# Kernel tuning notes

Measured on AMD Instinct MI355X. Metric: run time of the kernel, lower is better.

## Reference

```python
import jax, jax.numpy as jnp
import numpy as np

B, H, F, Z, T = 8192, 256, 128, 64, 43
STEPS = T - 3


def setup_inputs() -> dict:
    key = jax.random.key(0)
    ks = jax.random.split(key, 24)
    def nrm(k, shape, s=0.05):
        return (jax.random.normal(k, shape) * s).astype(jnp.float32)
    inp = {}
    inp["h_i"] = nrm(ks[0], (B, H), 1.0)                      # encoder context state
    t = jax.random.uniform(ks[1], (B, T)) * T                  # event timestamps, sorted
    inp["input_t"] = jnp.sort(t, axis=1).astype(jnp.float32)
    inp["eps_inf"] = jax.random.normal(ks[2], (STEPS, B, Z), dtype=jnp.float32)
    inp["eps_prior"] = jax.random.normal(ks[3], (STEPS, B, Z), dtype=jnp.float32)
    in_dim = Z + H + F
    inp["Wx"] = nrm(ks[4], (in_dim, 4 * H))
    inp["Wh"] = nrm(ks[5], (H, 4 * H))
    inp["b_lstm"] = jnp.zeros((4 * H,), jnp.float32)
    dims = [(H, F), (F, F), (F, F), (2 * H + 2 * F, Z), (Z, Z), (Z, Z), (2 * H + F, Z), (Z, Z), (Z, Z)]
    for i, (di, do) in enumerate(dims, 1):
        inp[f"w{i}"] = nrm(ks[5 + i], (di, do))
        inp[f"b{i}"] = jnp.zeros((do,), jnp.float32)
    inp["alpha"] = (jax.random.uniform(ks[20], (1, 1)) * 0.1).astype(jnp.float32)
    inp["beta"] = (jax.random.uniform(ks[21], (1, 1)) * 0.1).astype(jnp.float32)
    inp["mu0"] = (jax.random.uniform(ks[22], (1, 1)) * 0.1).astype(jnp.float32)
    return inp


def _forward(h_i, input_t, eps_inf, eps_prior, Wx, Wh, b_lstm,
             w1, b1, w2, b2, w3, b3, w4, b4, w5, b5, w6, b6, w7, b7, w8, b8, w9, b9,
             alpha, beta, mu0):
    batch = h_i.shape[0]
    idxs = jnp.arange(T)

    def dense(x, w, b):
        return jax.nn.relu(x @ w + b)

    def step(carry, xs):
        h, c, z_j, y_prev = carry
        e_i, e_p, j = xs
        # LSTM cell (Keras gate order i, f, c, o)
        x = jnp.concatenate([z_j, h_i, y_prev], axis=1)
        gates = x @ Wx + h @ Wh + b_lstm
        i_g, f_g, g_g, o_g = jnp.split(gates, 4, axis=1)
        c_new = jax.nn.sigmoid(f_g) * c + jax.nn.sigmoid(i_g) * jnp.tanh(g_g)
        h_new = jax.nn.sigmoid(o_g) * jnp.tanh(c_new)
        # Hawkes intensity over events strictly before current_time_index = j+3
        t_idx = j + 3
        t_cur = jnp.take(input_t, t_idx, axis=1)[:, None]          # [B,1]
        mask = idxs < t_idx                                         # [T]
        diff = jnp.where(mask[None, :], input_t - t_cur, -jnp.inf)
        trig = jnp.sum(jnp.exp(diff), axis=1, keepdims=True) * beta[0, 0]
        intensity = mu0[0, 0] + alpha[0, 0] * trig                  # [B,1]
        # original code gates state[1] (the cell state slot) with the intensity
        c_gated = intensity * c_new
        y = dense(dense(dense(h_new, w1, b1), w2, b2), w3, b3)
        # inference network (s_j = ungated c_new, mirroring the TF code)
        inf_in = jnp.concatenate([h_i, c_new, y, y_prev], axis=1)
        hz = dense(inf_in, w4, b4)
        mean_j = dense(hz, w5, b5)
        lv_j = dense(hz, w6, b6)
        z_new = mean_j + e_i * jnp.sqrt(jnp.exp(lv_j))
        # prior network
        pri_in = jnp.concatenate([h_i, c_new, y_prev], axis=1)
        hzp = dense(pri_in, w7, b7)
        mean_p = dense(hzp, w8, b8)
        lv_p = dense(hzp, w9, b9)
        z_p = mean_p + e_p * jnp.sqrt(jnp.exp(lv_p))
        return (h_new, c_gated, z_new, y), (y, mean_j, lv_j, z_new, z_p)

    carry0 = (jnp.zeros((batch, H), h_i.dtype), jnp.zeros((batch, H), h_i.dtype),
              jnp.zeros((batch, Z), h_i.dtype), jnp.zeros((batch, F), h_i.dtype))
    xs = (eps_inf, eps_prior, jnp.arange(STEPS))
    _, (ys, means, lvs, zs, zps) = jax.lax.scan(step, carry0, xs)
    # [STEPS,B,*] -> [B,STEPS,*]
    tr = lambda a: jnp.transpose(a, (1, 0, 2))
    return tr(ys), tr(means), tr(lvs), tr(zs), tr(zps)


def reference(h_i, input_t, eps_inf, eps_prior, Wx, Wh, b_lstm,
              w1, b1, w2, b2, w3, b3, w4, b4, w5, b5, w6, b6, w7, b7, w8, b8, w9, b9,
              alpha, beta, mu0):
    return _forward(h_i, input_t, eps_inf, eps_prior, Wx, Wh, b_lstm,
                    w1, b1, w2, b2, w3, b3, w4, b4, w5, b5, w6, b6, w7, b7, w8, b8, w9, b9,
                    alpha, beta, mu0)
```

## Files before the change

### kernel.cpp

```cpp
#include <hip/hip_runtime.h>


#define BDIM  8192
#define HDIM  256
#define FDIM  128
#define ZDIM  64
#define TDIM  43
#define STEPS 40

typedef __attribute__((ext_vector_type(8))) __bf16 bf16x8;
typedef __attribute__((ext_vector_type(4))) float  f32x4;

#define ACT_STRIDE 3248
#define C_Z   0
#define C_Y0  64
#define C_Y1  192
#define C_H0  320
#define C_H1  576
#define C_C   832
#define C_T0  1088
#define C_T1  1216
#define C_HZ  1344
#define C_HZP 1408
#define C_B4  1472
#define C_B7  1536

#define PW_GS  0u
#define PW_GHI 458752u
#define PW_W1  720896u
#define PW_W2  753664u
#define PW_W3  770048u
#define PW_W4S 786432u
#define PW_W4H 819200u
#define PW_W5  835584u
#define PW_W6  839680u
#define PW_W7S 843776u
#define PW_W7H 868352u
#define PW_W8  884736u
#define PW_W9  888832u

__device__ __forceinline__ int act_off(int row, int col) {
  return row * ACT_STRIDE + ((row >> 3) << 4) + (col << 1);
}
__device__ __forceinline__ f32x4 mfma16(bf16x8 a, bf16x8 b, f32x4 c) {
  return __builtin_amdgcn_mfma_f32_16x16x32_bf16(a, b, c, 0, 0, 0);
}
__device__ __forceinline__ float sigm(float x) { return 1.f / (1.f + __expf(-x)); }
__device__ __forceinline__ float tanh_f(float x) {
  float t = __expf(-2.f * fabsf(x));
  float r = (1.f - t) / (1.f + t);
  return x < 0.f ? -r : r;
}
__device__ __forceinline__ bf16x8 aread(const unsigned char* actb, int mt, int col,
                                        int lane) {
  return *(const bf16x8*)(actb + act_off(mt * 16 + (lane & 15), col + ((lane >> 4) << 3)));
}
__device__ __forceinline__ void st16(unsigned char* actb, int col, int mt, int rsub,
                                     f32x4 v, float bv) {
#pragma unroll
  for (int r = 0; r < 4; ++r)
    *(__bf16*)(actb + act_off(mt * 16 + rsub + r, col)) = (__bf16)fmaxf(v[r] + bv, 0.f);
}
__device__ __forceinline__ unsigned int pk2(float a, float b) {
  union { __bf16 h; unsigned short u; } x, y;
  x.h = (__bf16)a; y.h = (__bf16)b;
  return (unsigned int)x.u | ((unsigned int)y.u << 16);
}
__device__ __forceinline__ float upkf(unsigned int u, int hi) {
  union { unsigned int i; float f; } c;
  c.i = hi ? (u & 0xffff0000u) : (u << 16);
  return c.f;
}

struct PSeg { const float* p; int row0; int len; };

__global__ __launch_bounds__(256) void pack_w(PSeg s0, PSeg s1, PSeg s2,
                                              int K, int N, __bf16* __restrict__ dst) {
  int f = blockIdx.x * 256 + threadIdx.x;
  int KT = K >> 5;
  int total = KT * (N >> 4) * 64;
  if (f >= total) return;
  int lane = f & 63;
  int tile = f >> 6;
  int kt = tile % KT;
  int nt = tile / KT;
  int k0 = kt * 32 + ((lane >> 4) << 3);
  int n = (nt << 4) + (lane & 15);
  bf16x8 v;
#pragma unroll
  for (int j = 0; j < 8; ++j) {
    int k = k0 + j;
    const float* src;
    int r;
    if (k < s0.len) { src = s0.p; r = s0.row0 + k; }
    else if (k < s0.len + s1.len) { src = s1.p; r = s1.row0 + (k - s0.len); }
    else { src = s2.p; r = s2.row0 + (k - s0.len - s1.len); }
    v[j] = (__bf16)src[(size_t)r * N + n];
  }
  *(bf16x8*)(dst + (size_t)f * 8) = v;
}

struct Params {
  const float *h_i, *input_t, *eps_inf, *eps_prior;
  const float *b_lstm, *b1, *b2, *b3, *b4, *b5, *b6, *b7, *b8, *b9;
  const float *alpha, *beta, *mu0;
  const __bf16* wpack;
  float* out;
};

__global__ __launch_bounds__(1024, 4) void decoder_main(Params p) {
  __shared__ __align__(16) unsigned char act[32 * ACT_STRIDE];
  __shared__ float fbuf[2048];
  __shared__ float inten[STEPS * 32];

  const int tid = threadIdx.x;
  const int w = tid >> 6;
  const int lane = tid & 63;
  const int ln16 = lane & 15;
  const int rsub = (lane >> 4) << 2;
  const int r0 = blockIdx.x * 32;

  for (int i = tid; i < (32 * ACT_STRIDE) / 4; i += 1024) ((unsigned int*)act)[i] = 0u;
  __syncthreads();
  for (int i = tid; i < 32 * 256; i += 1024) {
    int row = i >> 8, col = i & 255;
    *(__bf16*)(act + act_off(row, C_C + col)) =
        (__bf16)p.h_i[(size_t)(r0 + row) * HDIM + col];
  }
  {
    float ab = p.alpha[0] * p.beta[0], mu = p.mu0[0];
    for (int t = tid; t < 32 * STEPS; t += 1024) {
      int row = t & 31, j = t >> 5;
      const float* tp = p.input_t + (size_t)(r0 + row) * TDIM;
      float tc = tp[j + 3];
      float s = 0.f;
      for (int idx = 0; idx < j + 3; ++idx) s += __expf(tp[idx] - tc);
      inten[j * 32 + row] = mu + ab * s;
    }
  }
  __syncthreads();

  const __bf16* W = p.wpack;
  const bf16x8* wgs = (const bf16x8*)(W + PW_GS);
  const bf16x8* wghi = (const bf16x8*)(W + PW_GHI);
  const bf16x8* w1p = (const bf16x8*)(W + PW_W1);
  const bf16x8* w2p = (const bf16x8*)(W + PW_W2);
  const bf16x8* w3p = (const bf16x8*)(W + PW_W3);
  const bf16x8* w4s = (const bf16x8*)(W + PW_W4S);
  const bf16x8* w4h = (const bf16x8*)(W + PW_W4H);
  const bf16x8* w5p = (const bf16x8*)(W + PW_W5);
  const bf16x8* w6p = (const bf16x8*)(W + PW_W6);
  const bf16x8* w7s = (const bf16x8*)(W + PW_W7S);
  const bf16x8* w7h = (const bf16x8*)(W + PW_W7H);
  const bf16x8* w8p = (const bf16x8*)(W + PW_W8);
  const bf16x8* w9p = (const bf16x8*)(W + PW_W9);

  uint2 gbp[4][2];
  {
    f32x4 g[4][2] = {};
#pragma unroll
    for (int kt = 0; kt < 8; ++kt) {
      bf16x8 a0 = aread(act, 0, C_C + kt * 32, lane);
      bf16x8 a1 = aread(act, 1, C_C + kt * 32, lane);
#pragma unroll
      for (int gg = 0; gg < 4; ++gg) {
        bf16x8 b = wghi[((size_t)(gg * 16 + w) * 8 + kt) * 64 + lane];
        g[gg][0] = mfma16(a0, b, g[gg][0]);
        g[gg][1] = mfma16(a1, b, g[gg][1]);
      }
    }
#pragma unroll
    for (int gg = 0; gg < 4; ++gg) {
      float bv = p.b_lstm[gg * 256 + w * 16 + ln16];
#pragma unroll
      for (int mt = 0; mt < 2; ++mt) {
        gbp[gg][mt].x = pk2(g[gg][mt][0] + bv, g[gg][mt][1] + bv);
        gbp[gg][mt].y = pk2(g[gg][mt][2] + bv, g[gg][mt][3] + bv);
      }
    }
  }
  {
    int n = w & 3, mt = (w >> 2) & 1;
    const bf16x8* wp = (w < 8) ? w4h : w7h;
    const float* bb = (w < 8) ? p.b4 : p.b7;
    int cb = (w < 8) ? C_B4 : C_B7;
    f32x4 v = {};
#pragma unroll
    for (int kt = 0; kt < 8; ++kt)
      v = mfma16(aread(act, mt, C_C + kt * 32, lane),
                 wp[(size_t)(n * 8 + kt) * 64 + lane], v);
    float bv = bb[n * 16 + ln16];
#pragma unroll
    for (int r = 0; r < 4; ++r)
      *(__bf16*)(act + act_off(mt * 16 + rsub + r, cb + n * 16 + ln16)) =
          (__bf16)(v[r] + bv);
  }
  f32x4 c_st[2] = {};
  __syncthreads();

  float* outy = p.out;
  float* outm = p.out + (size_t)BDIM * STEPS * FDIM;
  float* outl = outm + (size_t)BDIM * STEPS * ZDIM;
  float* outz = outl + (size_t)BDIM * STEPS * ZDIM;
  float* outzp = outz + (size_t)BDIM * STEPS * ZDIM;

  for (int j = 0; j < STEPS; ++j) {
    const int yW = (j & 1) ? C_Y1 : C_Y0, yR = (j & 1) ? C_Y0 : C_Y1;
    const int hW = (j & 1) ? C_H1 : C_H0, hR = (j & 1) ? C_H0 : C_H1;

    {
      f32x4 acc[4][2] = {};
#pragma unroll
      for (int kt = 0; kt < 14; ++kt) {
        int col = (kt < 2) ? (C_Z + kt * 32)
                           : (kt < 6) ? (yR + (kt - 2) * 32) : (hR + (kt - 6) * 32);
        bf16x8 a0 = aread(act, 0, col, lane);
        bf16x8 a1 = aread(act, 1, col, lane);
#pragma unroll
        for (int g = 0; g < 4; ++g) {
          bf16x8 b = wgs[((size_t)(g * 16 + w) * 14 + kt) * 64 + lane];
          acc[g][0] = mfma16(a0, b, acc[g][0]);
          acc[g][1] = mfma16(a1, b, acc[g][1]);
        }
      }
#pragma unroll
      for (int mt = 0; mt < 2; ++mt) {
#pragma unroll
        for (int r = 0; r < 4; ++r) {
          int row = mt * 16 + rsub + r;
          unsigned int ui = (r < 2) ? gbp[0][mt].x : gbp[0][mt].y;
          unsigned int uf = (r < 2) ? gbp[1][mt].x : gbp[1][mt].y;
          unsigned int ug = (r < 2) ? gbp[2][mt].x : gbp[2][mt].y;
          unsigned int uo = (r < 2) ? gbp[3][mt].x : gbp[3][mt].y;
          float ig = sigm(acc[0][mt][r] + upkf(ui, r & 1));
          float fg = sigm(acc[1][mt][r] + upkf(uf, r & 1));
          float gg = tanh_f(acc[2][mt][r] + upkf(ug, r & 1));
          float og = sigm(acc[3][mt][r] + upkf(uo, r & 1));
          float cn = fg * c_st[mt][r] + ig * gg;
          float hn = og * tanh_f(cn);
          c_st[mt][r] = inten[j * 32 + row] * cn;
          *(__bf16*)(act + act_off(row, C_C + w * 16 + ln16)) = (__bf16)cn;
          *(__bf16*)(act + act_off(row, hW + w * 16 + ln16)) = (__bf16)hn;
        }
      }
    }
    __syncthreads();

    if (w < 8) {
      f32x4 a0 = {}, a1 = {};
#pragma unroll
      for (int kt = 0; kt < 8; ++kt) {
        bf16x8 b = w1p[(size_t)(w * 8 + kt) * 64 + lane];
        a0 = mfma16(aread(act, 0, hW + kt * 32, lane), b, a0);
        a1 = mfma16(aread(act, 1, hW + kt * 32, lane), b, a1);
      }
      float bv = p.b1[w * 16 + ln16];
      st16(act, C_T0 + w * 16 + ln16, 0, rsub, a0, bv);
      st16(act, C_T0 + w * 16 + ln16, 1, rsub, a1, bv);
    } else {
      int n = w & 3, mt = (w >> 2) & 1;
      f32x4 v = {};
#pragma unroll
      for (int kt = 0; kt < 12; ++kt) {
        int col = (kt < 8) ? (C_C + kt * 32) : (yR + (kt - 8) * 32);
        v = mfma16(aread(act, mt, col, lane), w7s[(size_t)(n * 12 + kt) * 64 + lane], v);
      }
#pragma unroll
      for (int r = 0; r < 4; ++r) {
        int row = mt * 16 + rsub + r;
        float s = v[r] + (float)*(const __bf16*)(act + act_off(row, C_B7 + n * 16 + ln16));
        *(__bf16*)(act + act_off(row, C_HZP + n * 16 + ln16)) = (__bf16)fmaxf(s, 0.f);
      }
    }
    __syncthreads();

    if (w < 8) {
      f32x4 a0 = {}, a1 = {};
#pragma unroll
      for (int kt = 0; kt < 4; ++kt) {
        bf16x8 b = w2p[(size_t)(w * 4 + kt) * 64 + lane];
        a0 = mfma16(aread(act, 0, C_T0 + kt * 32, lane), b, a0);
        a1 = mfma16(aread(act, 1, C_T0 + kt * 32, lane), b, a1);
      }
      float bv = p.b2[w * 16 + ln16];
      st16(act, C_T1 + w * 16 + ln16, 0, rsub, a0, bv);
      st16(act, C_T1 + w * 16 + ln16, 1, rsub, a1, bv);
    } else {
      int n = w & 3, mt = (w >> 2) & 1;
      f32x4 vm = {}, vl = {};
#pragma unroll
      for (int kt = 0; kt < 2; ++kt) {
        bf16x8 a = aread(act, mt, C_HZP + kt * 32, lane);
        vm = mfma16(a, w8p[(size_t)(n * 2 + kt) * 64 + lane], vm);
        vl = mfma16(a, w9p[(size_t)(n * 2 + kt) * 64 + lane], vl);
      }
      float bm = p.b8[n * 16 + ln16], bl = p.b9[n * 16 + ln16];
#pragma unroll
      for (int r = 0; r < 4; ++r) {
        int row = mt * 16 + rsub + r, col = n * 16 + ln16;
        float mp = fmaxf(vm[r] + bm, 0.f), lp = fmaxf(vl[r] + bl, 0.f);
        float ep = __builtin_nontemporal_load(
            p.eps_prior + ((size_t)j * BDIM + r0 + row) * ZDIM + col);
        float zp = mp + ep * __expf(0.5f * lp);
        __builtin_nontemporal_store(
            zp, outzp + ((size_t)(r0 + row) * STEPS + j) * ZDIM + col);
      }
    }
    __syncthreads();

    if (w < 8) {
      f32x4 a0 = {}, a1 = {};
#pragma unroll
      for (int kt = 0; kt < 4; ++kt) {
        bf16x8 b = w3p[(size_t)(w * 4 + kt) * 64 + lane];
        a0 = mfma16(aread(act, 0, C_T1 + kt * 32, lane), b, a0);
        a1 = mfma16(aread(act, 1, C_T1 + kt * 32, lane), b, a1);
      }
      float bv = p.b3[w * 16 + ln16];
#pragma unroll
      for (int mt = 0; mt < 2; ++mt) {
        f32x4 vv = mt ? a1 : a0;
#pragma unroll
        for (int r = 0; r < 4; ++r) {
          int row = mt * 16 + rsub + r;
          float yv = fmaxf(vv[r] + bv, 0.f);
          *(__bf16*)(act + act_off(row, yW + w * 16 + ln16)) = (__bf16)yv;
          __builtin_nontemporal_store(
              yv, outy + ((size_t)(r0 + row) * STEPS + j) * FDIM + w * 16 + ln16);
        }
      }
    } else {
      int a = w - 8, n = a & 3, mt = a >> 2;
      f32x4 v = {};
#pragma unroll
      for (int kt = 0; kt < 8; ++kt)
        v = mfma16(aread(act, mt, C_C + kt * 32, lane),
                   w4s[(size_t)(n * 16 + kt) * 64 + lane], v);
#pragma unroll
      for (int kt = 12; kt < 16; ++kt)
        v = mfma16(aread(act, mt, yR + (kt - 12) * 32, lane),
                   w4s[(size_t)(n * 16 + kt) * 64 + lane], v);
#pragma unroll
      for (int r = 0; r < 4; ++r)
        fbuf[(mt * 16 + rsub + r) * 64 + n * 16 + ln16] = v[r];
    }
    __syncthreads();

    if (w < 8) {
      int n = w & 3, mt = w >> 2;
      f32x4 v = {};
#pragma unroll
      for (int kt = 8; kt < 12; ++kt)
        v = mfma16(aread(act, mt, yW + (kt - 8) * 32, lane),
                   w4s[(size_t)(n * 16 + kt) * 64 + lane], v);
#pragma unroll
      for (int r = 0; r < 4; ++r) {
        int row = mt * 16 + rsub + r, cc = n * 16 + ln16;
        float s = v[r] + fbuf[row * 64 + cc] +
                  (float)*(const __bf16*)(act + act_off(row, C_B4 + cc));
        *(__bf16*)(act + act_off(row, C_HZ + cc)) = (__bf16)fmaxf(s, 0.f);
      }
    }
    __syncthreads();

    if (w < 8) {
      int n = w & 3, mt = w >> 2;
      f32x4 vm = {}, vl = {};
#pragma unroll
      for (int kt = 0; kt < 2; ++kt) {
        bf16x8 a = aread(act, mt, C_HZ + kt * 32, lane);
        vm = mfma16(a, w5p[(size_t)(n * 2 + kt) * 64 + lane], vm);
        vl = mfma16(a, w6p[(size_t)(n * 2 + kt) * 64 + lane], vl);
      }
      float bm = p.b5[n * 16 + ln16], bl = p.b6[n * 16 + ln16];
#pragma unroll
      for (int r = 0; r < 4; ++r) {
        int row = mt * 16 + rsub + r, col = n * 16 + ln16;
        float m = fmaxf(vm[r] + bm, 0.f), l = fmaxf(vl[r] + bl, 0.f);
        float ei = __builtin_nontemporal_load(
            p.eps_inf + ((size_t)j * BDIM + r0 + row) * ZDIM + col);
        float zn = m + ei * __expf(0.5f * l);
        size_t ob = ((size_t)(r0 + row) * STEPS + j) * ZDIM + col;
        __builtin_nontemporal_store(m, outm + ob);
        __builtin_nontemporal_store(l, outl + ob);
        __builtin_nontemporal_store(zn, outz + ob);
        *(__bf16*)(act + act_off(row, C_Z + col)) = (__bf16)zn;
      }
    }
    __syncthreads();
  }
}

extern "C" void kernel_launch(void* const* d_in, const int* in_sizes, int n_in,
                              void* d_out, int out_size, void* d_ws, size_t ws_size,
                              hipStream_t stream) {
  const float* h_i = (const float*)d_in[0];
  const float* input_t = (const float*)d_in[1];
  const float* eps_inf = (const float*)d_in[2];
  const float* eps_prior = (const float*)d_in[3];
  const float* Wx = (const float*)d_in[4];
  const float* Wh = (const float*)d_in[5];
  const float* b_lstm = (const float*)d_in[6];
  const float* w1 = (const float*)d_in[7];  const float* b1 = (const float*)d_in[8];
  const float* w2 = (const float*)d_in[9];  const float* b2 = (const float*)d_in[10];
  const float* w3 = (const float*)d_in[11]; const float* b3 = (const float*)d_in[12];
  const float* w4 = (const float*)d_in[13]; const float* b4 = (const float*)d_in[14];
  const float* w5 = (const float*)d_in[15]; const float* b5 = (const float*)d_in[16];
  const float* w6 = (const float*)d_in[17]; const float* b6 = (const float*)d_in[18];
  const float* w7 = (const float*)d_in[19]; const float* b7 = (const float*)d_in[20];
  const float* w8 = (const float*)d_in[21]; const float* b8 = (const float*)d_in[22];
  const float* w9 = (const float*)d_in[23]; const float* b9 = (const float*)d_in[24];
  const float* alpha = (const float*)d_in[25];
  const float* beta = (const float*)d_in[26];
  const float* mu0 = (const float*)d_in[27];
  __bf16* ws = (__bf16*)d_ws;

  auto S = [](const float* ptr, int row0, int len) {
    PSeg s; s.p = ptr; s.row0 = row0; s.len = len; return s;
  };
  PSeg Zs; Zs.p = nullptr; Zs.row0 = 0; Zs.len = 0;
  auto L = [&](PSeg a, PSeg b, PSeg c, int K, int N, unsigned off) {
    int total = (K / 32) * (N / 16) * 64;
    pack_w<<<(total + 255) / 256, 256, 0, stream>>>(a, b, c, K, N, ws + off);
  };
  L(S(Wx, 0, 64), S(Wx, 320, 128), S(Wh, 0, 256), 448, 1024, PW_GS);
  L(S(Wx, 64, 256), Zs, Zs, 256, 1024, PW_GHI);
  L(S(w1, 0, 256), Zs, Zs, 256, 128, PW_W1);
  L(S(w2, 0, 128), Zs, Zs, 128, 128, PW_W2);
  L(S(w3, 0, 128), Zs, Zs, 128, 128, PW_W3);
  L(S(w4, 256, 512), Zs, Zs, 512, 64, PW_W4S);
  L(S(w4, 0, 256), Zs, Zs, 256, 64, PW_W4H);
  L(S(w5, 0, 64), Zs, Zs, 64, 64, PW_W5);
  L(S(w6, 0, 64), Zs, Zs, 64, 64, PW_W6);
  L(S(w7, 256, 384), Zs, Zs, 384, 64, PW_W7S);
  L(S(w7, 0, 256), Zs, Zs, 256, 64, PW_W7H);
  L(S(w8, 0, 64), Zs, Zs, 64, 64, PW_W8);
  L(S(w9, 0, 64), Zs, Zs, 64, 64, PW_W9);

  Params p;
  p.h_i = h_i; p.input_t = input_t; p.eps_inf = eps_inf; p.eps_prior = eps_prior;
  p.b_lstm = b_lstm; p.b1 = b1; p.b2 = b2; p.b3 = b3; p.b4 = b4; p.b5 = b5;
  p.b6 = b6; p.b7 = b7; p.b8 = b8; p.b9 = b9;
  p.alpha = alpha; p.beta = beta; p.mu0 = mu0;
  p.wpack = ws;
  p.out = (float*)d_out;

  decoder_main<<<256, 1024, 0, stream>>>(p);
}
```

Measured before the change: 2.687 ms.

## Stage packed weights through a double-buffered LDS ring and use 32x32 MFMA gates

Each step's weight matrices are now streamed cooperatively by the whole workgroup into a 64 KB double-buffered shared-memory ring, one slab at a time. This replaces per-wave direct global loads of packed weights, and it aims to cut redundant L2 traffic by loading each weight tile once per block. The LSTM gate GEMM now uses 32x32x16 MFMA over a full K of 704 on 8 waves, and the h_i contribution is recomputed every step instead of being precomputed once. The downstream dense layers are re-split across stages, with one barrier-separated phase per weight slab. The trade-off is many more workgroup barriers per step, extra gate FLOPs, and half the waves idle during the gate phase.

```diff
diff --git a/kernel.cpp b/kernel.cpp
--- a/kernel.cpp
+++ b/kernel.cpp
@@ -8,39 +8,43 @@
 #define TDIM  43
 #define STEPS 40
 
-typedef __attribute__((ext_vector_type(8))) __bf16 bf16x8;
-typedef __attribute__((ext_vector_type(4))) float  f32x4;
-
-#define ACT_STRIDE 3248
+typedef __attribute__((ext_vector_type(8)))  __bf16 bf16x8;
+typedef __attribute__((ext_vector_type(4)))  float  f32x4;
+typedef __attribute__((ext_vector_type(16))) float  f32x16;
+
+#define ACT_STRIDE 2704
 #define C_Z   0
-#define C_Y0  64
-#define C_Y1  192
-#define C_H0  320
-#define C_H1  576
+#define C_HI  64
+#define C_Y0  320
+#define C_Y1  448
+#define C_H   576
 #define C_C   832
 #define C_T0  1088
 #define C_T1  1216
-#define C_HZ  1344
-#define C_HZP 1408
-#define C_B4  1472
-#define C_B7  1536
-
-#define PW_GS  0u
-#define PW_GHI 458752u
-#define PW_W1  720896u
-#define PW_W2  753664u
-#define PW_W3  770048u
-#define PW_W4S 786432u
-#define PW_W4H 819200u
-#define PW_W5  835584u
-#define PW_W6  839680u
-#define PW_W7S 843776u
-#define PW_W7H 868352u
-#define PW_W8  884736u
-#define PW_W9  888832u
+#define C_HZP C_T0
+#define C_HZ  C_T1
+
+#define WB_G    0u
+#define WB_W1A  1441792u
+#define WB_W1B  1474560u
+#define WB_W2   1507328u
+#define WB_W3   1540096u
+#define WB_W7SA 1572864u
+#define WB_W7SB 1605632u
+#define WB_W4C  1622016u
+#define WB_W4YP 1654784u
+#define PW_W4H  843776u
+#define PW_W7H  860160u
+#define PW_W5   876544u
+#define PW_W6   880640u
+#define PW_W8   884736u
+#define PW_W9   888832u
 
 __device__ __forceinline__ int act_off(int row, int col) {
   return row * ACT_STRIDE + ((row >> 3) << 4) + (col << 1);
+}
+__device__ __forceinline__ f32x16 mfma32(bf16x8 a, bf16x8 b, f32x16 c) {
+  return __builtin_amdgcn_mfma_f32_32x32x16_bf16(a, b, c, 0, 0, 0);
 }
 __device__ __forceinline__ f32x4 mfma16(bf16x8 a, bf16x8 b, f32x4 c) {
   return __builtin_amdgcn_mfma_f32_16x16x32_bf16(a, b, c, 0, 0, 0);
@@ -51,52 +55,80 @@
   float r = (1.f - t) / (1.f + t);
   return x < 0.f ? -r : r;
 }
-__device__ __forceinline__ bf16x8 aread(const unsigned char* actb, int mt, int col,
-                                        int lane) {
-  return *(const bf16x8*)(actb + act_off(mt * 16 + (lane & 15), col + ((lane >> 4) << 3)));
-}
-__device__ __forceinline__ void st16(unsigned char* actb, int col, int mt, int rsub,
+__device__ __forceinline__ void wg_barrier() {
+  asm volatile("s_waitcnt lgkmcnt(0)" ::: "memory");
+  __builtin_amdgcn_s_barrier();
+  __builtin_amdgcn_sched_barrier(0);
+}
+struct StageReg { uint4 a, b; };
+__device__ __forceinline__ void issueS(StageReg& st, const unsigned char* src, int tid,
+                                       bool half) {
+  st.a = *(const uint4*)(src + tid * 16);
+  if (!half) st.b = *(const uint4*)(src + 16384 + tid * 16);
+}
+__device__ __forceinline__ void writeS(const StageReg& st, unsigned char* ring, int par,
+                                       int tid, bool half) {
+  *(uint4*)(ring + par * 32768 + tid * 16) = st.a;
+  if (!half) *(uint4*)(ring + par * 32768 + 16384 + tid * 16) = st.b;
+}
+__device__ __forceinline__ bf16x8 aread16(const unsigned char* a, int mt, int col,
+                                          int lane) {
+  return *(const bf16x8*)(a + act_off(mt * 16 + (lane & 15), col + ((lane >> 4) << 3)));
+}
+__device__ __forceinline__ bf16x8 aread32(const unsigned char* a, int col, int lane) {
+  return *(const bf16x8*)(a + act_off(lane & 31, col + ((lane >> 5) << 3)));
+}
+__device__ __forceinline__ void st16(unsigned char* a, int col, int mt, int rsub,
                                      f32x4 v, float bv) {
 #pragma unroll
   for (int r = 0; r < 4; ++r)
-    *(__bf16*)(actb + act_off(mt * 16 + rsub + r, col)) = (__bf16)fmaxf(v[r] + bv, 0.f);
-}
-__device__ __forceinline__ unsigned int pk2(float a, float b) {
-  union { __bf16 h; unsigned short u; } x, y;
-  x.h = (__bf16)a; y.h = (__bf16)b;
-  return (unsigned int)x.u | ((unsigned int)y.u << 16);
-}
-__device__ __forceinline__ float upkf(unsigned int u, int hi) {
-  union { unsigned int i; float f; } c;
-  c.i = hi ? (u & 0xffff0000u) : (u << 16);
-  return c.f;
-}
-
+    *(__bf16*)(a + act_off(mt * 16 + rsub + r, col)) = (__bf16)fmaxf(v[r] + bv, 0.f);
+}
+
+__global__ __launch_bounds__(256) void pack_gates(const float* __restrict__ Wx,
+                                                  const float* __restrict__ Wh,
+                                                  __bf16* __restrict__ dst) {
+  int f = blockIdx.x * 256 + threadIdx.x;
+  if (f >= 44 * 32 * 64) return;
+  int lane = f & 63, t = f >> 6, ct = t & 31, s = t >> 5;
+  int k0 = s * 16 + ((lane >> 5) << 3);
+  int col = (ct << 5) + (lane & 31);
+  bf16x8 v;
+#pragma unroll
+  for (int j = 0; j < 8; ++j) {
+    int k = k0 + j;
+    v[j] = (__bf16)((k < 448) ? Wx[(size_t)k * 1024 + col]
+                              : Wh[(size_t)(k - 448) * 1024 + col]);
+  }
+  *(bf16x8*)(dst + (size_t)f * 8) = v;
+}
+__global__ __launch_bounds__(256) void pack_tail(const float* __restrict__ src, int row0,
+                                                 int K, int N, __bf16* __restrict__ dst) {
+  int NT = N >> 4, KT = K >> 5;
+  int f = blockIdx.x * 256 + threadIdx.x;
+  if (f >= KT * NT * 64) return;
+  int lane = f & 63, t = f >> 6, nt = t % NT, kt = t / NT;
+  int k0 = row0 + kt * 32 + ((lane >> 4) << 3);
+  int col = (nt << 4) + (lane & 15);
+  bf16x8 v;
+#pragma unroll
+  for (int j = 0; j < 8; ++j) v[j] = (__bf16)src[(size_t)(k0 + j) * N + col];
+  *(bf16x8*)(dst + (size_t)f * 8) = v;
+}
 struct PSeg { const float* p; int row0; int len; };
-
-__global__ __launch_bounds__(256) void pack_w(PSeg s0, PSeg s1, PSeg s2,
-                                              int K, int N, __bf16* __restrict__ dst) {
-  int f = blockIdx.x * 256 + threadIdx.x;
+__global__ __launch_bounds__(256) void pack_w(PSeg s0, int K, int N,
+                                              __bf16* __restrict__ dst) {
   int KT = K >> 5;
   int total = KT * (N >> 4) * 64;
+  int f = blockIdx.x * 256 + threadIdx.x;
   if (f >= total) return;
-  int lane = f & 63;
-  int tile = f >> 6;
-  int kt = tile % KT;
-  int nt = tile / KT;
+  int lane = f & 63, tile = f >> 6, kt = tile % KT, nt = tile / KT;
   int k0 = kt * 32 + ((lane >> 4) << 3);
   int n = (nt << 4) + (lane & 15);
   bf16x8 v;
 #pragma unroll
-  for (int j = 0; j < 8; ++j) {
-    int k = k0 + j;
-    const float* src;
-    int r;
-    if (k < s0.len) { src = s0.p; r = s0.row0 + k; }
-    else if (k < s0.len + s1.len) { src = s1.p; r = s1.row0 + (k - s0.len); }
-    else { src = s2.p; r = s2.row0 + (k - s0.len - s1.len); }
-    v[j] = (__bf16)src[(size_t)r * N + n];
-  }
+  for (int j = 0; j < 8; ++j)
+    v[j] = (__bf16)s0.p[(size_t)(s0.row0 + k0 + j) * N + n];
   *(bf16x8*)(dst + (size_t)f * 8) = v;
 }
 
@@ -109,22 +141,24 @@
 };
 
 __global__ __launch_bounds__(1024, 4) void decoder_main(Params p) {
-  __shared__ __align__(16) unsigned char act[32 * ACT_STRIDE];
-  __shared__ float fbuf[2048];
+  __shared__ __align__(16) unsigned char act[86592];
+  __shared__ __align__(16) unsigned char ring[65536];
   __shared__ float inten[STEPS * 32];
 
   const int tid = threadIdx.x;
   const int w = tid >> 6;
   const int lane = tid & 63;
   const int ln16 = lane & 15;
+  const int nl = lane & 31;
   const int rsub = (lane >> 4) << 2;
   const int r0 = blockIdx.x * 32;
-
-  for (int i = tid; i < (32 * ACT_STRIDE) / 4; i += 1024) ((unsigned int*)act)[i] = 0u;
+  const unsigned char* wsb = (const unsigned char*)p.wpack;
+
+  for (int i = tid; i < 86592 / 4; i += 1024) ((unsigned int*)act)[i] = 0u;
   __syncthreads();
   for (int i = tid; i < 32 * 256; i += 1024) {
     int row = i >> 8, col = i & 255;
-    *(__bf16*)(act + act_off(row, C_C + col)) =
+    *(__bf16*)(act + act_off(row, C_HI + col)) =
         (__bf16)p.h_i[(size_t)(r0 + row) * HDIM + col];
   }
   {
@@ -141,61 +175,44 @@
   __syncthreads();
 
   const __bf16* W = p.wpack;
-  const bf16x8* wgs = (const bf16x8*)(W + PW_GS);
-  const bf16x8* wghi = (const bf16x8*)(W + PW_GHI);
-  const bf16x8* w1p = (const bf16x8*)(W + PW_W1);
-  const bf16x8* w2p = (const bf16x8*)(W + PW_W2);
-  const bf16x8* w3p = (const bf16x8*)(W + PW_W3);
-  const bf16x8* w4s = (const bf16x8*)(W + PW_W4S);
   const bf16x8* w4h = (const bf16x8*)(W + PW_W4H);
+  const bf16x8* w7h = (const bf16x8*)(W + PW_W7H);
   const bf16x8* w5p = (const bf16x8*)(W + PW_W5);
   const bf16x8* w6p = (const bf16x8*)(W + PW_W6);
-  const bf16x8* w7s = (const bf16x8*)(W + PW_W7S);
-  const bf16x8* w7h = (const bf16x8*)(W + PW_W7H);
   const bf16x8* w8p = (const bf16x8*)(W + PW_W8);
   const bf16x8* w9p = (const bf16x8*)(W + PW_W9);
 
-  uint2 gbp[4][2];
-  {
-    f32x4 g[4][2] = {};
+  const int n2 = (w & 7) & 3, m2 = ((w & 7) >> 2) & 1;
+  f32x4 b4f = {}, b7f = {};
+  if (w >= 8) {
+    f32x4 v4 = {}, v7 = {};
 #pragma unroll
     for (int kt = 0; kt < 8; ++kt) {
-      bf16x8 a0 = aread(act, 0, C_C + kt * 32, lane);
-      bf16x8 a1 = aread(act, 1, C_C + kt * 32, lane);
-#pragma unroll
-      for (int gg = 0; gg < 4; ++gg) {
-        bf16x8 b = wghi[((size_t)(gg * 16 + w) * 8 + kt) * 64 + lane];
-        g[gg][0] = mfma16(a0, b, g[gg][0]);
-        g[gg][1] = mfma16(a1, b, g[gg][1]);
-      }
-    }
-#pragma unroll
-    for (int gg = 0; gg < 4; ++gg) {
-      float bv = p.b_lstm[gg * 256 + w * 16 + ln16];
-#pragma unroll
-      for (int mt = 0; mt < 2; ++mt) {
-        gbp[gg][mt].x = pk2(g[gg][mt][0] + bv, g[gg][mt][1] + bv);
-        gbp[gg][mt].y = pk2(g[gg][mt][2] + bv, g[gg][mt][3] + bv);
-      }
-    }
+      bf16x8 a = aread16(act, m2, C_HI + kt * 32, lane);
+      v4 = mfma16(a, w4h[(size_t)(n2 * 8 + kt) * 64 + lane], v4);
+      v7 = mfma16(a, w7h[(size_t)(n2 * 8 + kt) * 64 + lane], v7);
+    }
+    float b4v = p.b4[n2 * 16 + ln16], b7v = p.b7[n2 * 16 + ln16];
+#pragma unroll
+    for (int r = 0; r < 4; ++r) { b4f[r] = v4[r] + b4v; b7f[r] = v7[r] + b7v; }
   }
-  {
-    int n = w & 3, mt = (w >> 2) & 1;
-    const bf16x8* wp = (w < 8) ? w4h : w7h;
-    const float* bb = (w < 8) ? p.b4 : p.b7;
-    int cb = (w < 8) ? C_B4 : C_B7;
-    f32x4 v = {};
-#pragma unroll
-    for (int kt = 0; kt < 8; ++kt)
-      v = mfma16(aread(act, mt, C_C + kt * 32, lane),
-                 wp[(size_t)(n * 8 + kt) * 64 + lane], v);
-    float bv = bb[n * 16 + ln16];
-#pragma unroll
-    for (int r = 0; r < 4; ++r)
-      *(__bf16*)(act + act_off(mt * 16 + rsub + r, cb + n * 16 + ln16)) =
-          (__bf16)(v[r] + bv);
+  float bA = 0, bB = 0;
+  float bi = 0, bf2 = 0, bg = 0, bo = 0, bv1 = 0, bv2 = 0, bv3 = 0;
+  if (w < 8) {
+    bA = p.b5[n2 * 16 + ln16];
+    bB = p.b6[n2 * 16 + ln16];
+    bi = p.b_lstm[w * 32 + nl];
+    bf2 = p.b_lstm[256 + w * 32 + nl];
+    bg = p.b_lstm[512 + w * 32 + nl];
+    bo = p.b_lstm[768 + w * 32 + nl];
+    bv1 = p.b1[w * 16 + ln16];
+    bv2 = p.b2[w * 16 + ln16];
+    bv3 = p.b3[w * 16 + ln16];
+  } else {
+    bA = p.b8[n2 * 16 + ln16];
+    bB = p.b9[n2 * 16 + ln16];
   }
-  f32x4 c_st[2] = {};
+  f32x16 c_st = {};
   __syncthreads();
 
   float* outy = p.out;
@@ -204,182 +221,236 @@
   float* outz = outl + (size_t)BDIM * STEPS * ZDIM;
   float* outzp = outz + (size_t)BDIM * STEPS * ZDIM;
 
+  StageReg st;
+  issueS(st, wsb + WB_G, tid, false);
+
   for (int j = 0; j < STEPS; ++j) {
     const int yW = (j & 1) ? C_Y1 : C_Y0, yR = (j & 1) ? C_Y0 : C_Y1;
-    const int hW = (j & 1) ? C_H1 : C_H0, hR = (j & 1) ? C_H0 : C_H1;
-
-    {
-      f32x4 acc[4][2] = {};
-#pragma unroll
-      for (int kt = 0; kt < 14; ++kt) {
-        int col = (kt < 2) ? (C_Z + kt * 32)
-                           : (kt < 6) ? (yR + (kt - 2) * 32) : (hR + (kt - 6) * 32);
-        bf16x8 a0 = aread(act, 0, col, lane);
-        bf16x8 a1 = aread(act, 1, col, lane);
-#pragma unroll
-        for (int g = 0; g < 4; ++g) {
-          bf16x8 b = wgs[((size_t)(g * 16 + w) * 14 + kt) * 64 + lane];
-          acc[g][0] = mfma16(a0, b, acc[g][0]);
-          acc[g][1] = mfma16(a1, b, acc[g][1]);
-        }
-      }
-#pragma unroll
-      for (int mt = 0; mt < 2; ++mt) {
-#pragma unroll
-        for (int r = 0; r < 4; ++r) {
-          int row = mt * 16 + rsub + r;
-          unsigned int ui = (r < 2) ? gbp[0][mt].x : gbp[0][mt].y;
-          unsigned int uf = (r < 2) ? gbp[1][mt].x : gbp[1][mt].y;
-          unsigned int ug = (r < 2) ? gbp[2][mt].x : gbp[2][mt].y;
-          unsigned int uo = (r < 2) ? gbp[3][mt].x : gbp[3][mt].y;
-          float ig = sigm(acc[0][mt][r] + upkf(ui, r & 1));
-          float fg = sigm(acc[1][mt][r] + upkf(uf, r & 1));
-          float gg = tanh_f(acc[2][mt][r] + upkf(ug, r & 1));
-          float og = sigm(acc[3][mt][r] + upkf(uo, r & 1));
-          float cn = fg * c_st[mt][r] + ig * gg;
-          float hn = og * tanh_f(cn);
-          c_st[mt][r] = inten[j * 32 + row] * cn;
-          *(__bf16*)(act + act_off(row, C_C + w * 16 + ln16)) = (__bf16)cn;
-          *(__bf16*)(act + act_off(row, hW + w * 16 + ln16)) = (__bf16)hn;
-        }
-      }
-    }
-    __syncthreads();
+
+    f32x16 a0 = {}, a1 = {}, a2 = {}, a3 = {};
+    for (int k = 0; k < 44; ++k) {
+      writeS(st, ring, k & 1, tid, false);
+      const unsigned char* nxt =
+          (k < 43) ? (wsb + WB_G + (unsigned)(k + 1) * 32768u) : (wsb + WB_W1A);
+      issueS(st, nxt, tid, false);
+      wg_barrier();
+      if (w < 8) {
+        const bf16x8* rb = (const bf16x8*)(ring + (k & 1) * 32768);
+        int colb = (k < 4) ? (C_Z + k * 16)
+                           : (k < 20) ? (C_HI + (k - 4) * 16)
+                                      : (k < 28) ? (yR + (k - 20) * 16)
+                                                 : (C_H + (k - 28) * 16);
+        bf16x8 a = aread32(act, colb, lane);
+        a0 = mfma32(a, rb[(0 * 8 + w) * 64 + lane], a0);
+        a1 = mfma32(a, rb[(1 * 8 + w) * 64 + lane], a1);
+        a2 = mfma32(a, rb[(2 * 8 + w) * 64 + lane], a2);
+        a3 = mfma32(a, rb[(3 * 8 + w) * 64 + lane], a3);
+      }
+      wg_barrier();
+    }
 
     if (w < 8) {
-      f32x4 a0 = {}, a1 = {};
-#pragma unroll
-      for (int kt = 0; kt < 8; ++kt) {
-        bf16x8 b = w1p[(size_t)(w * 8 + kt) * 64 + lane];
-        a0 = mfma16(aread(act, 0, hW + kt * 32, lane), b, a0);
-        a1 = mfma16(aread(act, 1, hW + kt * 32, lane), b, a1);
-      }
-      float bv = p.b1[w * 16 + ln16];
-      st16(act, C_T0 + w * 16 + ln16, 0, rsub, a0, bv);
-      st16(act, C_T0 + w * 16 + ln16, 1, rsub, a1, bv);
+#pragma unroll
+      for (int r = 0; r < 16; ++r) {
+        int row = (r & 3) + ((r >> 2) << 3) + ((lane >> 5) << 2);
+        float ig = sigm(a0[r] + bi);
+        float fg = sigm(a1[r] + bf2);
+        float gg = tanh_f(a2[r] + bg);
+        float og = sigm(a3[r] + bo);
+        float cn = fg * c_st[r] + ig * gg;
+        float hn = og * tanh_f(cn);
+        c_st[r] = inten[j * 32 + row] * cn;
+        *(__bf16*)(act + act_off(row, C_C + w * 32 + nl)) = (__bf16)cn;
+        *(__bf16*)(act + act_off(row, C_H + w * 32 + nl)) = (__bf16)hn;
+      }
+    }
+
+    writeS(st, ring, 0, tid, false);
+    issueS(st, wsb + WB_W1B, tid, false);
+    wg_barrier();
+    f32x4 y1a = {}, y1b = {};
+    if (w < 8) {
+      const bf16x8* rb = (const bf16x8*)(ring);
+#pragma unroll
+      for (int ktl = 0; ktl < 4; ++ktl) {
+        bf16x8 b = rb[(ktl * 8 + w) * 64 + lane];
+        y1a = mfma16(aread16(act, 0, C_H + ktl * 32, lane), b, y1a);
+        y1b = mfma16(aread16(act, 1, C_H + ktl * 32, lane), b, y1b);
+      }
+    }
+    wg_barrier();
+
+    writeS(st, ring, 1, tid, false);
+    issueS(st, wsb + WB_W2, tid, false);
+    wg_barrier();
+    if (w < 8) {
+      const bf16x8* rb = (const bf16x8*)(ring + 32768);
+#pragma unroll
+      for (int ktl = 0; ktl < 4; ++ktl) {
+        bf16x8 b = rb[(ktl * 8 + w) * 64 + lane];
+        y1a = mfma16(aread16(act, 0, C_H + (ktl + 4) * 32, lane), b, y1a);
+        y1b = mfma16(aread16(act, 1, C_H + (ktl + 4) * 32, lane), b, y1b);
+      }
+      st16(act, C_T0 + w * 16 + ln16, 0, rsub, y1a, bv1);
+      st16(act, C_T0 + w * 16 + ln16, 1, rsub, y1b, bv1);
+    }
+    wg_barrier();
+
+    writeS(st, ring, 0, tid, false);
+    issueS(st, wsb + WB_W3, tid, false);
+    wg_barrier();
+    bf16x8 w8f[2], w9f[2];
+    float ep[4];
+    if (w < 8) {
+      const bf16x8* rb = (const bf16x8*)(ring);
+      f32x4 c0 = {}, c1 = {};
+#pragma unroll
+      for (int ktl = 0; ktl < 4; ++ktl) {
+        bf16x8 b = rb[(ktl * 8 + w) * 64 + lane];
+        c0 = mfma16(aread16(act, 0, C_T0 + ktl * 32, lane), b, c0);
+        c1 = mfma16(aread16(act, 1, C_T0 + ktl * 32, lane), b, c1);
+      }
+      st16(act, C_T1 + w * 16 + ln16, 0, rsub, c0, bv2);
+      st16(act, C_T1 + w * 16 + ln16, 1, rsub, c1, bv2);
     } else {
-      int n = w & 3, mt = (w >> 2) & 1;
-      f32x4 v = {};
-#pragma unroll
-      for (int kt = 0; kt < 12; ++kt) {
-        int col = (kt < 8) ? (C_C + kt * 32) : (yR + (kt - 8) * 32);
-        v = mfma16(aread(act, mt, col, lane), w7s[(size_t)(n * 12 + kt) * 64 + lane], v);
+#pragma unroll
+      for (int kt = 0; kt < 2; ++kt) {
+        w8f[kt] = w8p[(size_t)(n2 * 2 + kt) * 64 + lane];
+        w9f[kt] = w9p[(size_t)(n2 * 2 + kt) * 64 + lane];
+      }
+#pragma unroll
+      for (int r = 0; r < 4; ++r)
+        ep[r] = p.eps_prior[((size_t)j * BDIM + r0 + m2 * 16 + rsub + r) * ZDIM +
+                            n2 * 16 + ln16];
+    }
+    wg_barrier();
+
+    writeS(st, ring, 1, tid, false);
+    issueS(st, wsb + WB_W7SA, tid, false);
+    wg_barrier();
+    if (w < 8) {
+      const bf16x8* rb = (const bf16x8*)(ring + 32768);
+      f32x4 c0 = {}, c1 = {};
+#pragma unroll
+      for (int ktl = 0; ktl < 4; ++ktl) {
+        bf16x8 b = rb[(ktl * 8 + w) * 64 + lane];
+        c0 = mfma16(aread16(act, 0, C_T1 + ktl * 32, lane), b, c0);
+        c1 = mfma16(aread16(act, 1, C_T1 + ktl * 32, lane), b, c1);
       }
 #pragma unroll
       for (int r = 0; r < 4; ++r) {
-        int row = mt * 16 + rsub + r;
-        float s = v[r] + (float)*(const __bf16*)(act + act_off(row, C_B7 + n * 16 + ln16));
-        *(__bf16*)(act + act_off(row, C_HZP + n * 16 + ln16)) = (__bf16)fmaxf(s, 0.f);
-      }
-    }
-    __syncthreads();
+        float yv0 = fmaxf(c0[r] + bv3, 0.f);
+        float yv1 = fmaxf(c1[r] + bv3, 0.f);
+        *(__bf16*)(act + act_off(rsub + r, yW + w * 16 + ln16)) = (__bf16)yv0;
+        *(__bf16*)(act + act_off(16 + rsub + r, yW + w * 16 + ln16)) = (__bf16)yv1;
+        __builtin_nontemporal_store(
+            yv0, outy + ((size_t)(r0 + rsub + r) * STEPS + j) * FDIM + w * 16 + ln16);
+        __builtin_nontemporal_store(
+            yv1,
+            outy + ((size_t)(r0 + 16 + rsub + r) * STEPS + j) * FDIM + w * 16 + ln16);
+      }
+    }
+    wg_barrier();
+
+    writeS(st, ring, 0, tid, false);
+    issueS(st, wsb + WB_W7SB, tid, true);
+    wg_barrier();
+    f32x4 hza = {};
+    bf16x8 w5f[2], w6f[2];
+    float ei[4];
+    if (w >= 8) {
+      const bf16x8* rb = (const bf16x8*)(ring);
+#pragma unroll
+      for (int ktl = 0; ktl < 8; ++ktl)
+        hza = mfma16(aread16(act, m2, C_C + ktl * 32, lane),
+                     rb[(ktl * 4 + n2) * 64 + lane], hza);
+    } else {
+#pragma unroll
+      for (int kt = 0; kt < 2; ++kt) {
+        w5f[kt] = w5p[(size_t)(n2 * 2 + kt) * 64 + lane];
+        w6f[kt] = w6p[(size_t)(n2 * 2 + kt) * 64 + lane];
+      }
+#pragma unroll
+      for (int r = 0; r < 4; ++r)
+        ei[r] = p.eps_inf[((size_t)j * BDIM + r0 + m2 * 16 + rsub + r) * ZDIM +
+                          n2 * 16 + ln16];
+    }
+    wg_barrier();
+
+    writeS(st, ring, 1, tid, true);
+    issueS(st, wsb + WB_W4C, tid, false);
+    wg_barrier();
+    if (w >= 8) {
+      const bf16x8* rb = (const bf16x8*)(ring + 32768);
+#pragma unroll
+      for (int ktl = 0; ktl < 4; ++ktl)
+        hza = mfma16(aread16(act, m2, yR + ktl * 32, lane),
+                     rb[(ktl * 4 + n2) * 64 + lane], hza);
+#pragma unroll
+      for (int r = 0; r < 4; ++r)
+        *(__bf16*)(act + act_off(m2 * 16 + rsub + r, C_HZP + n2 * 16 + ln16)) =
+            (__bf16)fmaxf(hza[r] + b7f[r], 0.f);
+    }
+    wg_barrier();
+
+    writeS(st, ring, 0, tid, false);
+    issueS(st, wsb + WB_W4YP, tid, false);
+    wg_barrier();
+    f32x4 vp = {};
+    if (w >= 8) {
+      const bf16x8* rb = (const bf16x8*)(ring);
+#pragma unroll
+      for (int ktl = 0; ktl < 8; ++ktl)
+        vp = mfma16(aread16(act, m2, C_C + ktl * 32, lane),
+                    rb[(ktl * 4 + n2) * 64 + lane], vp);
+      f32x4 vm = {}, vl = {};
+#pragma unroll
+      for (int ktl = 0; ktl < 2; ++ktl) {
+        bf16x8 a = aread16(act, m2, C_HZP + ktl * 32, lane);
+        vm = mfma16(a, w8f[ktl], vm);
+        vl = mfma16(a, w9f[ktl], vl);
+      }
+#pragma unroll
+      for (int r = 0; r < 4; ++r) {
+        float mp = fmaxf(vm[r] + bA, 0.f), lp = fmaxf(vl[r] + bB, 0.f);
+        float zp = mp + ep[r] * __expf(0.5f * lp);
+        __builtin_nontemporal_store(
+            zp, outzp + ((size_t)(r0 + m2 * 16 + rsub + r) * STEPS + j) * ZDIM +
+                    n2 * 16 + ln16);
+      }
+    }
+    wg_barrier();
+
+    writeS(st, ring, 1, tid, false);
+    issueS(st, wsb + WB_G, tid, false);
+    wg_barrier();
+    if (w >= 8) {
+      const bf16x8* rb = (const bf16x8*)(ring + 32768);
+#pragma unroll
+      for (int ktl = 0; ktl < 8; ++ktl) {
+        int col = (ktl < 4) ? (yW + ktl * 32) : (yR + (ktl - 4) * 32);
+        vp = mfma16(aread16(act, m2, col, lane), rb[(ktl * 4 + n2) * 64 + lane], vp);
+      }
+#pragma unroll
+      for (int r = 0; r < 4; ++r)
+        *(__bf16*)(act + act_off(m2 * 16 + rsub + r, C_HZ + n2 * 16 + ln16)) =
+            (__bf16)fmaxf(vp[r] + b4f[r], 0.f);
+    }
+    wg_barrier();
 
     if (w < 8) {
-      f32x4 a0 = {}, a1 = {};
-#pragma unroll
-      for (int kt = 0; kt < 4; ++kt) {
-        bf16x8 b = w2p[(size_t)(w * 4 + kt) * 64 + lane];
-        a0 = mfma16(aread(act, 0, C_T0 + kt * 32, lane), b, a0);
-        a1 = mfma16(aread(act, 1, C_T0 + kt * 32, lane), b, a1);
-      }
-      float bv = p.b2[w * 16 + ln16];
-      st16(act, C_T1 + w * 16 + ln16, 0, rsub, a0, bv);
-      st16(act, C_T1 + w * 16 + ln16, 1, rsub, a1, bv);
-    } else {
-      int n = w & 3, mt = (w >> 2) & 1;
       f32x4 vm = {}, vl = {};
 #pragma unroll
-      for (int kt = 0; kt < 2; ++kt) {
-        bf16x8 a = aread(act, mt, C_HZP + kt * 32, lane);
-        vm = mfma16(a, w8p[(size_t)(n * 2 + kt) * 64 + lane], vm);
-        vl = mfma16(a, w9p[(size_t)(n * 2 + kt) * 64 + lane], vl);
-      }
-      float bm = p.b8[n * 16 + ln16], bl = p.b9[n * 16 + ln16];
+      for (int ktl = 0; ktl < 2; ++ktl) {
+        bf16x8 a = aread16(act, m2, C_HZ + ktl * 32, lane);
+        vm = mfma16(a, w5f[ktl], vm);
+        vl = mfma16(a, w6f[ktl], vl);
+      }
 #pragma unroll
       for (int r = 0; r < 4; ++r) {
-        int row = mt * 16 + rsub + r, col = n * 16 + ln16;
-        float mp = fmaxf(vm[r] + bm, 0.f), lp = fmaxf(vl[r] + bl, 0.f);
-        float ep = __builtin_nontemporal_load(
-            p.eps_prior + ((size_t)j * BDIM + r0 + row) * ZDIM + col);
-        float zp = mp + ep * __expf(0.5f * lp);
-        __builtin_nontemporal_store(
-            zp, outzp + ((size_t)(r0 + row) * STEPS + j) * ZDIM + col);
-      }
-    }
-    __syncthreads();
-
-    if (w < 8) {
-      f32x4 a0 = {}, a1 = {};
-#pragma unroll
-      for (int kt = 0; kt < 4; ++kt) {
-        bf16x8 b = w3p[(size_t)(w * 4 + kt) * 64 + lane];
-        a0 = mfma16(aread(act, 0, C_T1 + kt * 32, lane), b, a0);
-        a1 = mfma16(aread(act, 1, C_T1 + kt * 32, lane), b, a1);
-      }
-      float bv = p.b3[w * 16 + ln16];
-#pragma unroll
-      for (int mt = 0; mt < 2; ++mt) {
-        f32x4 vv = mt ? a1 : a0;
-#pragma unroll
-        for (int r = 0; r < 4; ++r) {
-          int row = mt * 16 + rsub + r;
-          float yv = fmaxf(vv[r] + bv, 0.f);
-          *(__bf16*)(act + act_off(row, yW + w * 16 + ln16)) = (__bf16)yv;
-          __builtin_nontemporal_store(
-              yv, outy + ((size_t)(r0 + row) * STEPS + j) * FDIM + w * 16 + ln16);
-        }
-      }
-    } else {
-      int a = w - 8, n = a & 3, mt = a >> 2;
-      f32x4 v = {};
-#pragma unroll
-      for (int kt = 0; kt < 8; ++kt)
-        v = mfma16(aread(act, mt, C_C + kt * 32, lane),
-                   w4s[(size_t)(n * 16 + kt) * 64 + lane], v);
-#pragma unroll
-      for (int kt = 12; kt < 16; ++kt)
-        v = mfma16(aread(act, mt, yR + (kt - 12) * 32, lane),
-                   w4s[(size_t)(n * 16 + kt) * 64 + lane], v);
-#pragma unroll
-      for (int r = 0; r < 4; ++r)
-        fbuf[(mt * 16 + rsub + r) * 64 + n * 16 + ln16] = v[r];
-    }
-    __syncthreads();
-
-    if (w < 8) {
-      int n = w & 3, mt = w >> 2;
-      f32x4 v = {};
-#pragma unroll
-      for (int kt = 8; kt < 12; ++kt)
-        v = mfma16(aread(act, mt, yW + (kt - 8) * 32, lane),
-                   w4s[(size_t)(n * 16 + kt) * 64 + lane], v);
-#pragma unroll
-      for (int r = 0; r < 4; ++r) {
-        int row = mt * 16 + rsub + r, cc = n * 16 + ln16;
-        float s = v[r] + fbuf[row * 64 + cc] +
-                  (float)*(const __bf16*)(act + act_off(row, C_B4 + cc));
-        *(__bf16*)(act + act_off(row, C_HZ + cc)) = (__bf16)fmaxf(s, 0.f);
-      }
-    }
-    __syncthreads();
-
-    if (w < 8) {
-      int n = w & 3, mt = w >> 2;
-      f32x4 vm = {}, vl = {};
-#pragma unroll
-      for (int kt = 0; kt < 2; ++kt) {
-        bf16x8 a = aread(act, mt, C_HZ + kt * 32, lane);
-        vm = mfma16(a, w5p[(size_t)(n * 2 + kt) * 64 + lane], vm);
-        vl = mfma16(a, w6p[(size_t)(n * 2 + kt) * 64 + lane], vl);
-      }
-      float bm = p.b5[n * 16 + ln16], bl = p.b6[n * 16 + ln16];
-#pragma unroll
-      for (int r = 0; r < 4; ++r) {
-        int row = mt * 16 + rsub + r, col = n * 16 + ln16;
-        float m = fmaxf(vm[r] + bm, 0.f), l = fmaxf(vl[r] + bl, 0.f);
-        float ei = __builtin_nontemporal_load(
-            p.eps_inf + ((size_t)j * BDIM + r0 + row) * ZDIM + col);
-        float zn = m + ei * __expf(0.5f * l);
+        int row = m2 * 16 + rsub + r, col = n2 * 16 + ln16;
+        float m = fmaxf(vm[r] + bA, 0.f), l = fmaxf(vl[r] + bB, 0.f);
+        float zn = m + ei[r] * __expf(0.5f * l);
         size_t ob = ((size_t)(r0 + row) * STEPS + j) * ZDIM + col;
         __builtin_nontemporal_store(m, outm + ob);
         __builtin_nontemporal_store(l, outl + ob);
@@ -387,7 +458,6 @@
         *(__bf16*)(act + act_off(row, C_Z + col)) = (__bf16)zn;
       }
     }
-    __syncthreads();
   }
 }
 
@@ -415,27 +485,27 @@
   const float* mu0 = (const float*)d_in[27];
   __bf16* ws = (__bf16*)d_ws;
 
-  auto S = [](const float* ptr, int row0, int len) {
-    PSeg s; s.p = ptr; s.row0 = row0; s.len = len; return s;
+  pack_gates<<<(44 * 32 * 64 + 255) / 256, 256, 0, stream>>>(Wx, Wh, ws);
+  auto T = [&](const float* src, int row0, int K, int N, unsigned elem_off) {
+    int total = (K / 32) * (N / 16) * 64;
+    pack_tail<<<(total + 255) / 256, 256, 0, stream>>>(src, row0, K, N, ws + elem_off);
   };
-  PSeg Zs; Zs.p = nullptr; Zs.row0 = 0; Zs.len = 0;
-  auto L = [&](PSeg a, PSeg b, PSeg c, int K, int N, unsigned off) {
+  T(w1, 0, 256, 128, 720896u);
+  T(w2, 0, 128, 128, 753664u);
+  T(w3, 0, 128, 128, 770048u);
+  T(w7, 256, 384, 64, 786432u);
+  T(w4, 256, 512, 64, 811008u);
+  auto S = [&](const float* src, int row0, int K, int N, unsigned elem_off) {
+    PSeg s; s.p = src; s.row0 = row0; s.len = K;
     int total = (K / 32) * (N / 16) * 64;
-    pack_w<<<(total + 255) / 256, 256, 0, stream>>>(a, b, c, K, N, ws + off);
+    pack_w<<<(total + 255) / 256, 256, 0, stream>>>(s, K, N, ws + elem_off);
   };
-  L(S(Wx, 0, 64), S(Wx, 320, 128), S(Wh, 0, 256), 448, 1024, PW_GS);
-  L(S(Wx, 64, 256), Zs, Zs, 256, 1024, PW_GHI);
-  L(S(w1, 0, 256), Zs, Zs, 256, 128, PW_W1);
-  L(S(w2, 0, 128), Zs, Zs, 128, 128, PW_W2);
-  L(S(w3, 0, 128), Zs, Zs, 128, 128, PW_W3);
-  L(S(w4, 256, 512), Zs, Zs, 512, 64, PW_W4S);
-  L(S(w4, 0, 256), Zs, Zs, 256, 64, PW_W4H);
-  L(S(w5, 0, 64), Zs, Zs, 64, 64, PW_W5);
-  L(S(w6, 0, 64), Zs, Zs, 64, 64, PW_W6);
-  L(S(w7, 256, 384), Zs, Zs, 384, 64, PW_W7S);
-  L(S(w7, 0, 256), Zs, Zs, 256, 64, PW_W7H);
-  L(S(w8, 0, 64), Zs, Zs, 64, 64, PW_W8);
-  L(S(w9, 0, 64), Zs, Zs, 64, 64, PW_W9);
+  S(w4, 0, 256, 64, PW_W4H);
+  S(w7, 0, 256, 64, PW_W7H);
+  S(w5, 0, 64, 64, PW_W5);
+  S(w6, 0, 64, 64, PW_W6);
+  S(w8, 0, 64, 64, PW_W8);
+  S(w9, 0, 64, 64, PW_W9);
 
   Params p;
   p.h_i = h_i; p.input_t = input_t; p.eps_inf = eps_inf; p.eps_prior = eps_prior;
```

Result: slower. 5.993 ms (+123.0%).
